# Kernel optimization log

Hardware: AMD Instinct MI355X
Metric: run time of the kernel (lower is better)

The kernel has to match this reference:

```python
import jax, jax.numpy as jnp
import numpy as np

EPS = 1e-5
NUM_HEADS = 16

def layernorm(x, g, b):
    mu = jnp.mean(x, axis=-1, keepdims=True)
    var = jnp.mean(jnp.square(x - mu), axis=-1, keepdims=True)
    return (x - mu) * jax.lax.rsqrt(var + EPS) * g + b

def setup_inputs() -> dict:
    key = jax.random.key(0)
    ks = jax.random.split(key, 5)
    B, N, C = 2, 2048, 1024
    s_in = 1.0 / np.sqrt(C)
    return {
        "x": jax.random.normal(ks[0], (B, N, C), jnp.float32),
        "ln1_g": jnp.ones((C,), jnp.float32),
        "ln1_b": jnp.zeros((C,), jnp.float32),
        "w_qk": jax.random.normal(ks[1], (C, 2 * C), jnp.float32) * s_in,
        "w_v": jax.random.normal(ks[2], (C, C), jnp.float32) * s_in,
        "ln2_g": jnp.ones((C,), jnp.float32),
        "ln2_b": jnp.zeros((C,), jnp.float32),
        "w_proj": jax.random.normal(ks[3], (C, C), jnp.float32) * s_in,
        "b_proj": jnp.zeros((C,), jnp.float32),
    }

def reference(x, ln1_g, ln1_b, w_qk, w_v, ln2_g, ln2_b, w_proj, b_proj):
    B, N, C = x.shape
    H = NUM_HEADS
    hd = C // H
    scale = hd ** (-0.5)
    xn = layernorm(x, ln1_g, ln1_b)
    # qk: [B,N,2C] -> q,k each [B,H,N,hd]
    qk = (xn @ w_qk).reshape(B, N, 2, H, hd).transpose(2, 0, 3, 1, 4)
    q, k = qk[0], qk[1]
    v = (xn @ w_v).reshape(B, N, H, hd).transpose(0, 2, 1, 3)  # [B,H,N,hd]
    attn = jnp.einsum("bhqd,bhkd->bhqk", q, k) * scale
    attn = jax.nn.softmax(attn, axis=-1)
    out = jnp.einsum("bhqk,bhkd->bhqd", attn, v)  # [B,H,N,hd]
    out = out.transpose(0, 2, 1, 3).reshape(B, N, C)
    out = layernorm(out, ln2_g, ln2_b)
    return out @ w_proj + b_proj
```

## Files before the change

### kernel.cpp

```cpp
#include <hip/hip_runtime.h>
#include <hip/hip_bf16.h>


typedef __attribute__((ext_vector_type(8))) short short8;
typedef __attribute__((ext_vector_type(4))) short short4v;
typedef __attribute__((ext_vector_type(4))) float float4v;
typedef __attribute__((ext_vector_type(4))) unsigned uint4v;

__device__ __forceinline__ unsigned short f2bf(float f) {
    unsigned u = __builtin_bit_cast(unsigned, f);
    return (unsigned short)((u + 0x7FFFu + ((u >> 16) & 1u)) >> 16);
}
__device__ __forceinline__ unsigned cvtpk(float lo, float hi) {
    unsigned r;
    asm("v_cvt_pk_bf16_f32 %0, %1, %2" : "=v"(r) : "v"(lo), "v"(hi));
    return r;
}
__device__ __forceinline__ void gll16(const unsigned short* g, unsigned short* l) {
    __builtin_amdgcn_global_load_lds(
        (const __attribute__((address_space(1))) unsigned int*)g,
        (__attribute__((address_space(3))) unsigned int*)l, 16, 0, 0);
}

__global__ __launch_bounds__(256) void prep(
    const float* __restrict__ x, const float* __restrict__ g1, const float* __restrict__ b1,
    const float* __restrict__ w_qk, const float* __restrict__ w_v,
    const float* __restrict__ w_proj, const float* __restrict__ g2,
    const float* __restrict__ b2,
    unsigned short* __restrict__ xn, unsigned short* __restrict__ wqkvT,
    unsigned short* __restrict__ wgT, float* __restrict__ u, float* __restrict__ w0) {
    __shared__ float sh[32 * 33];
    const int bid = blockIdx.x, tid = threadIdx.x;
    if (bid < 1024) {
        const int lane = tid & 63;
        const int row = bid * 4 + (tid >> 6);
        const float4* xr = reinterpret_cast<const float4*>(x + (size_t)row * 1024);
        const float4* G4 = reinterpret_cast<const float4*>(g1);
        const float4* B4 = reinterpret_cast<const float4*>(b1);
        float4 v[4];
        float s = 0.f, sq = 0.f;
#pragma unroll
        for (int i = 0; i < 4; i++) {
            v[i] = xr[i * 64 + lane];
            s  += (v[i].x + v[i].y) + (v[i].z + v[i].w);
            sq += (v[i].x * v[i].x + v[i].y * v[i].y) + (v[i].z * v[i].z + v[i].w * v[i].w);
        }
#pragma unroll
        for (int off = 32; off >= 1; off >>= 1) {
            s  += __shfl_xor(s, off, 64);
            sq += __shfl_xor(sq, off, 64);
        }
        const float mu = s * (1.f / 1024.f);
        const float rstd = rsqrtf(sq * (1.f / 1024.f) - mu * mu + 1e-5f);
#pragma unroll
        for (int i = 0; i < 4; i++) {
            const float4 gv = G4[i * 64 + lane], bv = B4[i * 64 + lane];
            ushort4 o;
            o.x = f2bf((v[i].x - mu) * rstd * gv.x + bv.x);
            o.y = f2bf((v[i].y - mu) * rstd * gv.y + bv.y);
            o.z = f2bf((v[i].z - mu) * rstd * gv.z + bv.z);
            o.w = f2bf((v[i].w - mu) * rstd * gv.w + bv.w);
            *reinterpret_cast<ushort4*>(&xn[(size_t)row * 1024 + i * 256 + lane * 4]) = o;
        }
    } else {
        const float* in; unsigned short* out; int Cc, bx, by; bool doU = false;
        if (bid < 3072)      { int t = bid - 1024; in = w_qk;   out = wqkvT;               Cc = 2048; bx = t & 63; by = t >> 6; }
        else if (bid < 4096) { int t = bid - 3072; in = w_v;    out = wqkvT + 2048 * 1024; Cc = 1024; bx = t & 31; by = t >> 5; }
        else                 { int t = bid - 4096; in = w_proj; out = wgT; doU = true;     Cc = 1024; bx = t & 31; by = t >> 5; }
        const int c0 = bx * 32, r0 = by * 32;
        const int tx = tid & 31, ty = tid >> 5;
#pragma unroll
        for (int i = 0; i < 32; i += 8)
            sh[(ty + i) * 33 + tx] = in[(size_t)(r0 + ty + i) * Cc + c0 + tx];
        __syncthreads();
        const float scale = doU ? g2[r0 + tx] : 1.f;
        const float b2v   = doU ? b2[r0 + tx] : 0.f;
#pragma unroll
        for (int i = 0; i < 32; i += 8) {
            const float raw = sh[tx * 33 + ty + i];
            const float sc  = raw * scale;
            out[(size_t)(c0 + ty + i) * 1024 + r0 + tx] = f2bf(sc);
            if (doU) {
                float pu = sc, pw = raw * b2v;
#pragma unroll
                for (int off = 1; off <= 16; off <<= 1) {
                    pu += __shfl_xor(pu, off, 64);
                    pw += __shfl_xor(pw, off, 64);
                }
                if (tx == 0) {
                    atomicAdd(&u[c0 + ty + i], pu);
                    atomicAdd(&w0[c0 + ty + i], pw);
                }
            }
        }
    }
}

__global__ __launch_bounds__(512, 2) void gemm_qkv(const unsigned short* __restrict__ A,
                                                   const unsigned short* __restrict__ Bt,
                                                   unsigned short* __restrict__ qb,
                                                   unsigned short* __restrict__ kb,
                                                   unsigned short* __restrict__ vT) {
    __shared__ unsigned short As[2 * 128 * 64];
    __shared__ unsigned short Bs[2 * 192 * 64];
    const int tid = threadIdx.x, lane = tid & 63, w = tid >> 6;
    const int wm = (w >> 2) * 64, wn = (w & 3) * 48;
    const int quad = lane >> 4, l16 = lane & 15;
    const int ls = lane >> 3, sg = lane & 7;
    const int m0 = blockIdx.y * 128, n0 = blockIdx.x * 192;

    float4v acc[4][3];
#pragma unroll
    for (int mi = 0; mi < 4; mi++)
#pragma unroll
        for (int ni = 0; ni < 3; ni++) acc[mi][ni] = float4v{0.f, 0.f, 0.f, 0.f};

    const int g = (sg ^ ls) * 8;
#pragma unroll
    for (int i = 0; i < 2; i++)
        gll16(&A[(size_t)(m0 + w * 16 + i * 8 + ls) * 1024 + g], &As[(w * 16 + i * 8) * 64]);
#pragma unroll
    for (int i = 0; i < 3; i++)
        gll16(&Bt[(size_t)(n0 + w * 24 + i * 8 + ls) * 1024 + g], &Bs[(w * 24 + i * 8) * 64]);

#pragma unroll 1
    for (int s = 0; s < 16; s++) {
        __syncthreads();
        if (s + 1 < 16) {
            const int k0 = (s + 1) << 6;
            unsigned short* Ad = As + (((s + 1) & 1) << 13);
            unsigned short* Bd = Bs + (((s + 1) & 1) * 12288);
#pragma unroll
            for (int i = 0; i < 2; i++)
                gll16(&A[(size_t)(m0 + w * 16 + i * 8 + ls) * 1024 + k0 + g],
                      &Ad[(w * 16 + i * 8) * 64]);
#pragma unroll
            for (int i = 0; i < 3; i++)
                gll16(&Bt[(size_t)(n0 + w * 24 + i * 8 + ls) * 1024 + k0 + g],
                      &Bd[(w * 24 + i * 8) * 64]);
        }
        const unsigned short* Ac = As + ((s & 1) << 13);
        const unsigned short* Bc = Bs + ((s & 1) * 12288);
#pragma unroll
        for (int ks = 0; ks < 2; ks++) {
            short8 af[4], bfr[3];
#pragma unroll
            for (int mi = 0; mi < 4; mi++) {
                const int r = wm + mi * 16 + l16;
                af[mi] = *reinterpret_cast<const short8*>(
                    &Ac[r * 64 + ((ks * 4 + quad) ^ (r & 7)) * 8]);
            }
#pragma unroll
            for (int ni = 0; ni < 3; ni++) {
                const int r = wn + ni * 16 + l16;
                bfr[ni] = *reinterpret_cast<const short8*>(
                    &Bc[r * 64 + ((ks * 4 + quad) ^ (r & 7)) * 8]);
            }
#pragma unroll
            for (int mi = 0; mi < 4; mi++)
#pragma unroll
                for (int ni = 0; ni < 3; ni++)
                    acc[mi][ni] = __builtin_amdgcn_mfma_f32_16x16x32_bf16(
                        af[mi], bfr[ni], acc[mi][ni], 0, 0, 0);
        }
    }

    const float QSCALE = 0.125f * 1.4426950408889634f;
#pragma unroll
    for (int mi = 0; mi < 4; mi++) {
        const int row0 = m0 + wm + mi * 16 + quad * 4;
        const int b = row0 >> 11, nq = row0 & 2047;
#pragma unroll
        for (int ni = 0; ni < 3; ni++) {
            const int col = n0 + wn + ni * 16 + l16;
            if (col < 1024) {
                const int h = col >> 6, d = col & 63;
#pragma unroll
                for (int r = 0; r < 4; r++)
                    qb[(((size_t)b * 16 + h) * 2048 + nq + r) * 64 + d] =
                        f2bf(acc[mi][ni][r] * QSCALE);
            } else if (col < 2048) {
                const int c = col - 1024, h = c >> 6, d = c & 63;
#pragma unroll
                for (int r = 0; r < 4; r++)
                    kb[(((size_t)b * 16 + h) * 2048 + nq + r) * 64 + d] = f2bf(acc[mi][ni][r]);
            } else {
                const int c = col - 2048, h = c >> 6, d = c & 63;
                const short4v sv = {(short)f2bf(acc[mi][ni][0]), (short)f2bf(acc[mi][ni][1]),
                                    (short)f2bf(acc[mi][ni][2]), (short)f2bf(acc[mi][ni][3])};
                *reinterpret_cast<short4v*>(
                    &vT[(((size_t)b * 16 + h) * 64 + d) * 2048 + nq]) = sv;
            }
        }
    }
}

__global__ __launch_bounds__(512, 4) void flash_attn(const unsigned short* __restrict__ qbuf,
                                                     const unsigned short* __restrict__ kb,
                                                     const unsigned short* __restrict__ vT,
                                                     unsigned short* __restrict__ attn,
                                                     float2* __restrict__ part) {
    __shared__ __align__(16) unsigned short KB[2][2][64 * 64];
    __shared__ __align__(16) unsigned short VB[2][2][64 * 64];
    __shared__ float lsh[4][2][64];
    const int tid = threadIdx.x, lane = tid & 63, w = tid >> 6;
    const int wq = w & 3, kh = w >> 2;
    const int quad = lane >> 4, l16 = lane & 15;
    const int ls = lane >> 3, sg = lane & 7;
    const int bh = blockIdx.x, q0 = blockIdx.y * 128;
    const size_t nbase = (size_t)bh * 2048;

    const int pr = w * 8 + ls;
    const int srow = (pr & 32) | ((pr & 12) << 1) | ((pr & 16) >> 2) | (pr & 3);
    const int sgran = (sg ^ ls) << 3;

    short8 bq[2][2];
#pragma unroll
    for (int q2 = 0; q2 < 2; q2++)
#pragma unroll
        for (int ks = 0; ks < 2; ks++)
            bq[q2][ks] = *reinterpret_cast<const short8*>(
                &qbuf[(nbase + q0 + wq * 32 + q2 * 16 + l16) * 64 + ks * 32 + quad * 8]);

    float l_part[2] = {0.f, 0.f};
    float4v o_acc[2][4];
#pragma unroll
    for (int q2 = 0; q2 < 2; q2++)
#pragma unroll
        for (int db = 0; db < 4; db++) o_acc[q2][db] = float4v{0.f, 0.f, 0.f, 0.f};

#define FSTAGE(t, buf)                                                                  \
    _Pragma("unroll")                                                                   \
    for (int t2 = 0; t2 < 2; t2++) {                                                    \
        gll16(&kb[(nbase + (t) * 128 + t2 * 64 + srow) * 64 + sgran],                   \
              &KB[buf][t2][w * 8 * 64]);                                                \
        gll16(&vT[((size_t)bh * 64 + w * 8 + ls) * 2048 + (t) * 128 + t2 * 64 + sgran], \
              &VB[buf][t2][w * 8 * 64]);                                                \
    }

    FSTAGE(0, 0);

#pragma unroll 1
    for (int s = 0; s < 16; s++) {
        __syncthreads();
        if (s + 1 < 16) FSTAGE(s + 1, (s + 1) & 1);

#pragma unroll
        for (int t2 = 0; t2 < 2; t2++) {
            const unsigned short* Kc = KB[s & 1][t2];
            const unsigned short* Vc = VB[s & 1][t2];

            short8 kf[2][2];
#pragma unroll
            for (int ks = 0; ks < 2; ks++)
#pragma unroll
                for (int cc = 0; cc < 2; cc++) {
                    const int r = kh * 32 + cc * 16 + l16;
                    kf[ks][cc] = *reinterpret_cast<const short8*>(
                        &Kc[r * 64 + ((ks * 4 + quad) ^ (r & 7)) * 8]);
                }
            short8 va[4];
#pragma unroll
            for (int db = 0; db < 4; db++) {
                const int r = db * 16 + l16;
                va[db] = *reinterpret_cast<const short8*>(
                    &Vc[r * 64 + ((kh * 4 + quad) ^ (r & 7)) * 8]);
            }

#pragma unroll
            for (int q2 = 0; q2 < 2; q2++) {
                float4v s_acc[2];
#pragma unroll
                for (int cc = 0; cc < 2; cc++) s_acc[cc] = float4v{0.f, 0.f, 0.f, 0.f};
                __builtin_amdgcn_s_setprio(1);
#pragma unroll
                for (int ks = 0; ks < 2; ks++)
#pragma unroll
                    for (int cc = 0; cc < 2; cc++)
                        s_acc[cc] = __builtin_amdgcn_mfma_f32_16x16x32_bf16(
                            kf[ks][cc], bq[q2][ks], s_acc[cc], 0, 0, 0);
                __builtin_amdgcn_s_setprio(0);

                float ls2 = 0.f;
                float p[8];
#pragma unroll
                for (int cc = 0; cc < 2; cc++)
#pragma unroll
                    for (int r = 0; r < 4; r++) {
                        const float pv = __builtin_amdgcn_exp2f(s_acc[cc][r]);
                        p[cc * 4 + r] = pv;
                        ls2 += pv;
                    }
                uint4v pd;
                pd.x = cvtpk(p[0], p[1]); pd.y = cvtpk(p[2], p[3]);
                pd.z = cvtpk(p[4], p[5]); pd.w = cvtpk(p[6], p[7]);
                const short8 pb = __builtin_bit_cast(short8, pd);
                l_part[q2] += ls2;
                __builtin_amdgcn_s_setprio(1);
#pragma unroll
                for (int db = 0; db < 4; db++)
                    o_acc[q2][db] = __builtin_amdgcn_mfma_f32_16x16x32_bf16(
                        va[db], pb, o_acc[q2][db], 0, 0, 0);
                __builtin_amdgcn_s_setprio(0);
            }
        }
    }
#undef FSTAGE

    __syncthreads();
    float* osh = reinterpret_cast<float*>(KB);
    const int swz = (l16 & 7) << 2;
    if (kh == 1) {
#pragma unroll
        for (int q2 = 0; q2 < 2; q2++)
#pragma unroll
            for (int db = 0; db < 4; db++) {
                const int base = (wq * 32 + q2 * 16 + l16) * 64 + db * 16 + quad * 4;
                *reinterpret_cast<float4v*>(&osh[base ^ swz]) = o_acc[q2][db];
            }
        lsh[wq][0][lane] = l_part[0];
        lsh[wq][1][lane] = l_part[1];
    }
    __syncthreads();
    if (kh == 0) {
        const int b = bh >> 4, h = bh & 15;
#pragma unroll
        for (int q2 = 0; q2 < 2; q2++) {
            float lr = l_part[q2] + lsh[wq][q2][lane];
            lr += __shfl_xor(lr, 16, 64);
            lr += __shfl_xor(lr, 32, 64);
            const float inv = 1.f / lr;
            const int grow = b * 2048 + q0 + wq * 32 + q2 * 16 + l16;
            float sum = 0.f, s2 = 0.f;
#pragma unroll
            for (int db = 0; db < 4; db++) {
                const int base = (wq * 32 + q2 * 16 + l16) * 64 + db * 16 + quad * 4;
                const float4v oh = *reinterpret_cast<const float4v*>(&osh[base ^ swz]);
                const float o0 = (o_acc[q2][db][0] + oh[0]) * inv;
                const float o1 = (o_acc[q2][db][1] + oh[1]) * inv;
                const float o2 = (o_acc[q2][db][2] + oh[2]) * inv;
                const float o3 = (o_acc[q2][db][3] + oh[3]) * inv;
                const ushort4 st = {f2bf(o0), f2bf(o1), f2bf(o2), f2bf(o3)};
                *reinterpret_cast<ushort4*>(
                    &attn[(size_t)grow * 1024 + h * 64 + db * 16 + quad * 4]) = st;
                sum += (o0 + o1) + (o2 + o3);
                s2  += (o0 * o0 + o1 * o1) + (o2 * o2 + o3 * o3);
            }
            sum += __shfl_xor(sum, 16, 64); sum += __shfl_xor(sum, 32, 64);
            s2  += __shfl_xor(s2, 16, 64);  s2  += __shfl_xor(s2, 32, 64);
            if (quad == 0) part[(size_t)grow * 16 + h] = float2{sum, s2};
        }
    }
}

__global__ __launch_bounds__(256) void gemm_proj(const unsigned short* __restrict__ A,
                                                 const unsigned short* __restrict__ Bt,
                                                 const float2* __restrict__ part,
                                                 const float* __restrict__ u,
                                                 const float* __restrict__ w0,
                                                 const float* __restrict__ bias,
                                                 float* __restrict__ out) {
    __shared__ unsigned short As[2 * 128 * 64];
    __shared__ unsigned short Bs[2 * 64 * 64];
    __shared__ float2 rstat_s[128];
    const int tid = threadIdx.x, lane = tid & 63, w = tid >> 6;
    const int quad = lane >> 4, l16 = lane & 15;
    const int ls = lane >> 3, sg = lane & 7;
    const int m0 = blockIdx.y * 128, n0 = blockIdx.x * 64;
    {
        const int rloc = tid >> 1, half = tid & 1;
        const float4* p4 = reinterpret_cast<const float4*>(part);
        float s = 0.f, s2 = 0.f;
#pragma unroll
        for (int j = 0; j < 4; j++) {
            const float4 p = p4[(size_t)(m0 + rloc) * 8 + half * 4 + j];
            s += p.x + p.z; s2 += p.y + p.w;
        }
        s  += __shfl_xor(s, 1, 64);
        s2 += __shfl_xor(s2, 1, 64);
        if (!half) {
            const float mu = s * (1.f / 1024.f);
            const float rstd = rsqrtf(s2 * (1.f / 1024.f) - mu * mu + 1e-5f);
            rstat_s[rloc] = float2{rstd, mu * rstd};
        }
    }

    float4v acc[2][4];
#pragma unroll
    for (int mi = 0; mi < 2; mi++)
#pragma unroll
        for (int ni = 0; ni < 4; ni++) acc[mi][ni] = float4v{0.f, 0.f, 0.f, 0.f};

    const int g = (sg ^ ls) * 8;
#pragma unroll
    for (int i = 0; i < 4; i++)
        gll16(&A[(size_t)(m0 + w * 32 + i * 8 + ls) * 1024 + g], &As[(w * 32 + i * 8) * 64]);
#pragma unroll
    for (int i = 0; i < 2; i++)
        gll16(&Bt[(size_t)(n0 + w * 16 + i * 8 + ls) * 1024 + g], &Bs[(w * 16 + i * 8) * 64]);

#pragma unroll 1
    for (int s = 0; s < 16; s++) {
        __syncthreads();
        if (s + 1 < 16) {
            const int k0 = (s + 1) << 6;
            unsigned short* Ad = As + (((s + 1) & 1) << 13);
            unsigned short* Bd = Bs + (((s + 1) & 1) << 12);
#pragma unroll
            for (int i = 0; i < 4; i++)
                gll16(&A[(size_t)(m0 + w * 32 + i * 8 + ls) * 1024 + k0 + g],
                      &Ad[(w * 32 + i * 8) * 64]);
#pragma unroll
            for (int i = 0; i < 2; i++)
                gll16(&Bt[(size_t)(n0 + w * 16 + i * 8 + ls) * 1024 + k0 + g],
                      &Bd[(w * 16 + i * 8) * 64]);
        }
        const unsigned short* Ac = As + ((s & 1) << 13);
        const unsigned short* Bc = Bs + ((s & 1) << 12);
#pragma unroll
        for (int ks = 0; ks < 2; ks++) {
            short8 af[2], bfr[4];
#pragma unroll
            for (int mi = 0; mi < 2; mi++) {
                const int r = w * 32 + mi * 16 + l16;
                af[mi] = *reinterpret_cast<const short8*>(
                    &Ac[r * 64 + ((ks * 4 + quad) ^ (r & 7)) * 8]);
            }
#pragma unroll
            for (int ni = 0; ni < 4; ni++) {
                const int r = ni * 16 + l16;
                bfr[ni] = *reinterpret_cast<const short8*>(
                    &Bc[r * 64 + ((ks * 4 + quad) ^ (r & 7)) * 8]);
            }
#pragma unroll
            for (int mi = 0; mi < 2; mi++)
#pragma unroll
                for (int ni = 0; ni < 4; ni++)
                    acc[mi][ni] = __builtin_amdgcn_mfma_f32_16x16x32_bf16(
                        af[mi], bfr[ni], acc[mi][ni], 0, 0, 0);
        }
    }

#pragma unroll
    for (int mi = 0; mi < 2; mi++) {
        const int rl0 = w * 32 + mi * 16 + quad * 4;
        float2 rs[4];
#pragma unroll
        for (int r = 0; r < 4; r++) rs[r] = rstat_s[rl0 + r];
#pragma unroll
        for (int ni = 0; ni < 4; ni++) {
            const int col = n0 + ni * 16 + l16;
            const float uu = u[col], ww = w0[col] + bias[col];
#pragma unroll
            for (int r = 0; r < 4; r++)
                out[(size_t)(m0 + rl0 + r) * 1024 + col] =
                    fmaf(rs[r].x, acc[mi][ni][r], ww - rs[r].y * uu);
        }
    }
}

extern "C" void kernel_launch(void* const* d_in, const int* in_sizes, int n_in,
                              void* d_out, int out_size, void* d_ws, size_t ws_size,
                              hipStream_t stream) {
    const float* x      = (const float*)d_in[0];
    const float* ln1_g  = (const float*)d_in[1];
    const float* ln1_b  = (const float*)d_in[2];
    const float* w_qk   = (const float*)d_in[3];
    const float* w_v    = (const float*)d_in[4];
    const float* ln2_g  = (const float*)d_in[5];
    const float* ln2_b  = (const float*)d_in[6];
    const float* w_proj = (const float*)d_in[7];
    const float* b_proj = (const float*)d_in[8];
    float* out = (float*)d_out;

    char* ws = (char*)d_ws;
    unsigned short* xn      = (unsigned short*)(ws + 0);
    unsigned short* wqkvT   = (unsigned short*)(ws + 8388608);
    unsigned short* wgT     = (unsigned short*)(ws + 14680064);
    unsigned short* qbuf    = (unsigned short*)(ws + 16777216);
    unsigned short* kbuf    = (unsigned short*)(ws + 25165824);
    unsigned short* vTbuf   = (unsigned short*)(ws + 33554432);
    unsigned short* attn    = (unsigned short*)(ws + 41943040);
    float2*         part    = (float2*)(ws + 50331648);
    float*          u       = (float*)(ws + 50888704);
    float*          w0      = (float*)(ws + 50892800);

    hipMemsetAsync(ws + 50888704, 0, 8192, stream);
    prep<<<5120, 256, 0, stream>>>(x, ln1_g, ln1_b, w_qk, w_v, w_proj, ln2_g, ln2_b,
                                   xn, wqkvT, wgT, u, w0);
    gemm_qkv<<<dim3(16, 32), 512, 0, stream>>>(xn, wqkvT, qbuf, kbuf, vTbuf);
    flash_attn<<<dim3(32, 16), 512, 0, stream>>>(qbuf, kbuf, vTbuf, attn, part);
    gemm_proj<<<dim3(16, 32), 256, 0, stream>>>(attn, wgT, part, u, w0, b_proj, out);
}
```

Measured before the change: 186.8 us.

## Use 4-wave flash attention blocks with 64 query rows per wave

The flash attention kernel drops from 8 waves to 4 waves per block. Each wave now owns 64 query rows instead of 32, so every K/V fragment loaded from LDS feeds four query tiles rather than two. The KV tile shrinks to 64 keys per stage, which doubles the number of pipeline stages and barriers. The aim is to cut LDS read traffic per MFMA, at the cost of more registers per wave, possibly lower occupancy, and fewer waves available to hide latency.

```diff
diff --git a/kernel.cpp b/kernel.cpp
--- a/kernel.cpp
+++ b/kernel.cpp
@@ -195,146 +195,149 @@
     }
 }
 
-__global__ __launch_bounds__(512, 4) void flash_attn(const unsigned short* __restrict__ qbuf,
-                                                     const unsigned short* __restrict__ kb,
-                                                     const unsigned short* __restrict__ vT,
-                                                     unsigned short* __restrict__ attn,
-                                                     float2* __restrict__ part) {
-    __shared__ __align__(16) unsigned short KB[2][2][64 * 64];
-    __shared__ __align__(16) unsigned short VB[2][2][64 * 64];
-    __shared__ float lsh[4][2][64];
+__global__ __launch_bounds__(256) void flash_attn(const unsigned short* __restrict__ qbuf,
+                                                  const unsigned short* __restrict__ kb,
+                                                  const unsigned short* __restrict__ vT,
+                                                  unsigned short* __restrict__ attn,
+                                                  float2* __restrict__ part) {
+    __shared__ __align__(16) unsigned short KV[4][64 * 64];
+    __shared__ float lsh[2][4][64];
     const int tid = threadIdx.x, lane = tid & 63, w = tid >> 6;
-    const int wq = w & 3, kh = w >> 2;
+    const int wq = w & 1, kh = w >> 1;
     const int quad = lane >> 4, l16 = lane & 15;
     const int ls = lane >> 3, sg = lane & 7;
     const int bh = blockIdx.x, q0 = blockIdx.y * 128;
     const size_t nbase = (size_t)bh * 2048;
 
-    const int pr = w * 8 + ls;
-    const int srow = (pr & 32) | ((pr & 12) << 1) | ((pr & 16) >> 2) | (pr & 3);
+    int srow[2];
+#pragma unroll
+    for (int i = 0; i < 2; i++) {
+        const int pr = w * 16 + i * 8 + ls;
+        srow[i] = (pr & 32) | ((pr & 12) << 1) | ((pr & 16) >> 2) | (pr & 3);
+    }
     const int sgran = (sg ^ ls) << 3;
 
-    short8 bq[2][2];
-#pragma unroll
-    for (int q2 = 0; q2 < 2; q2++)
+    short8 bq[4][2];
+#pragma unroll
+    for (int q2 = 0; q2 < 4; q2++)
 #pragma unroll
         for (int ks = 0; ks < 2; ks++)
             bq[q2][ks] = *reinterpret_cast<const short8*>(
-                &qbuf[(nbase + q0 + wq * 32 + q2 * 16 + l16) * 64 + ks * 32 + quad * 8]);
-
-    float l_part[2] = {0.f, 0.f};
-    float4v o_acc[2][4];
-#pragma unroll
-    for (int q2 = 0; q2 < 2; q2++)
+                &qbuf[(nbase + q0 + wq * 64 + q2 * 16 + l16) * 64 + ks * 32 + quad * 8]);
+
+    float l_part[4] = {0.f, 0.f, 0.f, 0.f};
+    float4v o_acc[4][4];
+#pragma unroll
+    for (int q2 = 0; q2 < 4; q2++)
 #pragma unroll
         for (int db = 0; db < 4; db++) o_acc[q2][db] = float4v{0.f, 0.f, 0.f, 0.f};
 
-#define FSTAGE(t, buf)                                                                  \
-    _Pragma("unroll")                                                                   \
-    for (int t2 = 0; t2 < 2; t2++) {                                                    \
-        gll16(&kb[(nbase + (t) * 128 + t2 * 64 + srow) * 64 + sgran],                   \
-              &KB[buf][t2][w * 8 * 64]);                                                \
-        gll16(&vT[((size_t)bh * 64 + w * 8 + ls) * 2048 + (t) * 128 + t2 * 64 + sgran], \
-              &VB[buf][t2][w * 8 * 64]);                                                \
-    }
-
-    FSTAGE(0, 0);
+#pragma unroll
+    for (int i = 0; i < 2; i++) {
+        gll16(&kb[(nbase + srow[i]) * 64 + sgran], &KV[0][(w * 16 + i * 8) * 64]);
+        gll16(&vT[((size_t)bh * 64 + w * 16 + i * 8 + ls) * 2048 + sgran],
+              &KV[2][(w * 16 + i * 8) * 64]);
+    }
 
 #pragma unroll 1
-    for (int s = 0; s < 16; s++) {
+    for (int s = 0; s < 32; s++) {
         __syncthreads();
-        if (s + 1 < 16) FSTAGE(s + 1, (s + 1) & 1);
-
-#pragma unroll
-        for (int t2 = 0; t2 < 2; t2++) {
-            const unsigned short* Kc = KB[s & 1][t2];
-            const unsigned short* Vc = VB[s & 1][t2];
-
-            short8 kf[2][2];
+        if (s + 1 < 32) {
+            const int ktn = (s + 1) << 6, buf = (s + 1) & 1;
+#pragma unroll
+            for (int i = 0; i < 2; i++) {
+                gll16(&kb[(nbase + ktn + srow[i]) * 64 + sgran],
+                      &KV[buf][(w * 16 + i * 8) * 64]);
+                gll16(&vT[((size_t)bh * 64 + w * 16 + i * 8 + ls) * 2048 + ktn + sgran],
+                      &KV[2 + buf][(w * 16 + i * 8) * 64]);
+            }
+        }
+        const unsigned short* Kc = KV[s & 1];
+        const unsigned short* Vc = KV[2 + (s & 1)];
+
+        short8 kf[2][2];
+#pragma unroll
+        for (int ks = 0; ks < 2; ks++)
+#pragma unroll
+            for (int cc = 0; cc < 2; cc++) {
+                const int r = kh * 32 + cc * 16 + l16;
+                kf[ks][cc] = *reinterpret_cast<const short8*>(
+                    &Kc[r * 64 + ((ks * 4 + quad) ^ (r & 7)) * 8]);
+            }
+        short8 va[4];
+#pragma unroll
+        for (int db = 0; db < 4; db++) {
+            const int r = db * 16 + l16;
+            va[db] = *reinterpret_cast<const short8*>(
+                &Vc[r * 64 + ((kh * 4 + quad) ^ (r & 7)) * 8]);
+        }
+
+#pragma unroll
+        for (int q2 = 0; q2 < 4; q2++) {
+            float4v s_acc[2];
+#pragma unroll
+            for (int cc = 0; cc < 2; cc++) s_acc[cc] = float4v{0.f, 0.f, 0.f, 0.f};
+            __builtin_amdgcn_s_setprio(1);
 #pragma unroll
             for (int ks = 0; ks < 2; ks++)
 #pragma unroll
-                for (int cc = 0; cc < 2; cc++) {
-                    const int r = kh * 32 + cc * 16 + l16;
-                    kf[ks][cc] = *reinterpret_cast<const short8*>(
-                        &Kc[r * 64 + ((ks * 4 + quad) ^ (r & 7)) * 8]);
+                for (int cc = 0; cc < 2; cc++)
+                    s_acc[cc] = __builtin_amdgcn_mfma_f32_16x16x32_bf16(
+                        kf[ks][cc], bq[q2][ks], s_acc[cc], 0, 0, 0);
+            __builtin_amdgcn_s_setprio(0);
+
+            float ls2 = 0.f;
+            float p[8];
+#pragma unroll
+            for (int cc = 0; cc < 2; cc++)
+#pragma unroll
+                for (int r = 0; r < 4; r++) {
+                    const float pv = __builtin_amdgcn_exp2f(s_acc[cc][r]);
+                    p[cc * 4 + r] = pv;
+                    ls2 += pv;
                 }
-            short8 va[4];
-#pragma unroll
-            for (int db = 0; db < 4; db++) {
-                const int r = db * 16 + l16;
-                va[db] = *reinterpret_cast<const short8*>(
-                    &Vc[r * 64 + ((kh * 4 + quad) ^ (r & 7)) * 8]);
-            }
-
-#pragma unroll
-            for (int q2 = 0; q2 < 2; q2++) {
-                float4v s_acc[2];
-#pragma unroll
-                for (int cc = 0; cc < 2; cc++) s_acc[cc] = float4v{0.f, 0.f, 0.f, 0.f};
-                __builtin_amdgcn_s_setprio(1);
-#pragma unroll
-                for (int ks = 0; ks < 2; ks++)
-#pragma unroll
-                    for (int cc = 0; cc < 2; cc++)
-                        s_acc[cc] = __builtin_amdgcn_mfma_f32_16x16x32_bf16(
-                            kf[ks][cc], bq[q2][ks], s_acc[cc], 0, 0, 0);
-                __builtin_amdgcn_s_setprio(0);
-
-                float ls2 = 0.f;
-                float p[8];
-#pragma unroll
-                for (int cc = 0; cc < 2; cc++)
-#pragma unroll
-                    for (int r = 0; r < 4; r++) {
-                        const float pv = __builtin_amdgcn_exp2f(s_acc[cc][r]);
-                        p[cc * 4 + r] = pv;
-                        ls2 += pv;
-                    }
-                uint4v pd;
-                pd.x = cvtpk(p[0], p[1]); pd.y = cvtpk(p[2], p[3]);
-                pd.z = cvtpk(p[4], p[5]); pd.w = cvtpk(p[6], p[7]);
-                const short8 pb = __builtin_bit_cast(short8, pd);
-                l_part[q2] += ls2;
-                __builtin_amdgcn_s_setprio(1);
-#pragma unroll
-                for (int db = 0; db < 4; db++)
-                    o_acc[q2][db] = __builtin_amdgcn_mfma_f32_16x16x32_bf16(
-                        va[db], pb, o_acc[q2][db], 0, 0, 0);
-                __builtin_amdgcn_s_setprio(0);
-            }
-        }
-    }
-#undef FSTAGE
+            uint4v pd;
+            pd.x = cvtpk(p[0], p[1]); pd.y = cvtpk(p[2], p[3]);
+            pd.z = cvtpk(p[4], p[5]); pd.w = cvtpk(p[6], p[7]);
+            const short8 pb = __builtin_bit_cast(short8, pd);
+            l_part[q2] += ls2;
+            __builtin_amdgcn_s_setprio(1);
+#pragma unroll
+            for (int db = 0; db < 4; db++)
+                o_acc[q2][db] = __builtin_amdgcn_mfma_f32_16x16x32_bf16(
+                    va[db], pb, o_acc[q2][db], 0, 0, 0);
+            __builtin_amdgcn_s_setprio(0);
+        }
+    }
 
     __syncthreads();
-    float* osh = reinterpret_cast<float*>(KB);
+    float* osh = reinterpret_cast<float*>(KV);
     const int swz = (l16 & 7) << 2;
     if (kh == 1) {
 #pragma unroll
-        for (int q2 = 0; q2 < 2; q2++)
+        for (int q2 = 0; q2 < 4; q2++) {
 #pragma unroll
             for (int db = 0; db < 4; db++) {
-                const int base = (wq * 32 + q2 * 16 + l16) * 64 + db * 16 + quad * 4;
+                const int base = (wq * 64 + q2 * 16 + l16) * 64 + db * 16 + quad * 4;
                 *reinterpret_cast<float4v*>(&osh[base ^ swz]) = o_acc[q2][db];
             }
-        lsh[wq][0][lane] = l_part[0];
-        lsh[wq][1][lane] = l_part[1];
+            lsh[wq][q2][lane] = l_part[q2];
+        }
     }
     __syncthreads();
     if (kh == 0) {
         const int b = bh >> 4, h = bh & 15;
 #pragma unroll
-        for (int q2 = 0; q2 < 2; q2++) {
+        for (int q2 = 0; q2 < 4; q2++) {
             float lr = l_part[q2] + lsh[wq][q2][lane];
             lr += __shfl_xor(lr, 16, 64);
             lr += __shfl_xor(lr, 32, 64);
             const float inv = 1.f / lr;
-            const int grow = b * 2048 + q0 + wq * 32 + q2 * 16 + l16;
+            const int grow = b * 2048 + q0 + wq * 64 + q2 * 16 + l16;
             float sum = 0.f, s2 = 0.f;
 #pragma unroll
             for (int db = 0; db < 4; db++) {
-                const int base = (wq * 32 + q2 * 16 + l16) * 64 + db * 16 + quad * 4;
+                const int base = (wq * 64 + q2 * 16 + l16) * 64 + db * 16 + quad * 4;
                 const float4v oh = *reinterpret_cast<const float4v*>(&osh[base ^ swz]);
                 const float o0 = (o_acc[q2][db][0] + oh[0]) * inv;
                 const float o1 = (o_acc[q2][db][1] + oh[1]) * inv;
@@ -489,6 +492,6 @@
     prep<<<5120, 256, 0, stream>>>(x, ln1_g, ln1_b, w_qk, w_v, w_proj, ln2_g, ln2_b,
                                    xn, wqkvT, wgT, u, w0);
     gemm_qkv<<<dim3(16, 32), 512, 0, stream>>>(xn, wqkvT, qbuf, kbuf, vTbuf);
-    flash_attn<<<dim3(32, 16), 512, 0, stream>>>(qbuf, kbuf, vTbuf, attn, part);
+    flash_attn<<<dim3(32, 16), 256, 0, stream>>>(qbuf, kbuf, vTbuf, attn, part);
     gemm_proj<<<dim3(16, 32), 256, 0, stream>>>(attn, wgT, part, u, w0, b_proj, out);
 }
```

Result: slower. 193.4 us (+3.5%).
